# Kernel optimization log

Measured on AMD Instinct MI355X. Metric: run time of the kernel, lower is better.

## Reference

```python
import jax, jax.numpy as jnp
import numpy as np

COST_BBOX = 1.0
COST_GIOU = 1.0
TOPK = 5


def _make_boxes(key, b, n):
    # valid xyxy boxes in [0,1]: centers + small positive sizes
    kc, ks = jax.random.split(key)
    cxy = jax.random.uniform(kc, (b, n, 2))
    wh = jax.random.uniform(ks, (b, n, 2)) * 0.2 + 0.01
    return jnp.concatenate([cxy - wh / 2, cxy + wh / 2], axis=-1)


def setup_inputs() -> dict:
    key = jax.random.key(0)
    k1, k2, k3, k4 = jax.random.split(key, 4)
    B, NP, NG = 8, 5000, 300
    return {
        "pred_box": _make_boxes(k1, B, NP),
        "pred_obj": jax.random.normal(k3, (B, NP), dtype=jnp.float32),
        "gt_box": _make_boxes(k2, B, NG),
        "gt_obj": jax.random.normal(k4, (B, NG), dtype=jnp.float32),
    }


def pairwise_giou(pb, gb):
    # pb: [B,N,4], gb: [B,M,4] in xyxy -> giou [B,N,M]
    area_p = (pb[..., 2] - pb[..., 0]) * (pb[..., 3] - pb[..., 1])  # [B,N]
    area_g = (gb[..., 2] - gb[..., 0]) * (gb[..., 3] - gb[..., 1])  # [B,M]
    lt = jnp.maximum(pb[:, :, None, :2], gb[:, None, :, :2])  # [B,N,M,2]
    rb = jnp.minimum(pb[:, :, None, 2:], gb[:, None, :, 2:])
    wh = jnp.clip(rb - lt, 0.0)
    inter = wh[..., 0] * wh[..., 1]                                  # [B,N,M]
    union = area_p[:, :, None] + area_g[:, None, :] - inter
    iou = inter / union
    # smallest enclosing box
    lt_e = jnp.minimum(pb[:, :, None, :2], gb[:, None, :, :2])
    rb_e = jnp.maximum(pb[:, :, None, 2:], gb[:, None, :, 2:])
    wh_e = jnp.clip(rb_e - lt_e, 0.0)
    area_e = wh_e[..., 0] * wh_e[..., 1]
    return iou - (area_e - union) / area_e


def cost_matrix(pred_box, gt_box):
    # L1 cdist: [B,N,M]
    cost_bbox = jnp.sum(jnp.abs(pred_box[:, :, None, :] - gt_box[:, None, :, :]), axis=-1)
    cost_giou = 1.0 - pairwise_giou(pred_box, gt_box)
    return COST_BBOX * cost_bbox + COST_GIOU * cost_giou


def reference(pred_box, pred_obj, gt_box, gt_obj):
    C = cost_matrix(pred_box, gt_box)            # [B, N_pred, N_gt]
    Ct = jnp.swapaxes(C, 1, 2)                   # [B, N_gt, N_pred]
    _, idx = jax.lax.top_k(-Ct, TOPK)            # smallest-cost preds per gt: [B, N_gt, TOPK]
    B, M, _ = idx.shape
    matched_pred = idx.reshape(B, M * TOPK).astype(jnp.int32)
    matched_gt = jnp.broadcast_to(jnp.repeat(jnp.arange(M, dtype=jnp.int32), TOPK)[None, :], (B, M * TOPK))
    return matched_pred, matched_gt
```

## Files before the change

kernel.cpp:

```cpp
#include <hip/hip_runtime.h>

#pragma clang fp contract(off)

typedef unsigned long long u64;
typedef float f4 __attribute__((ext_vector_type(4)));

#define TOPK 5
#define WAVES 4

#define CE(x, y) do { const u64 _a = (x), _b = (y); const bool _l = _b < _a; \
                      (x) = _l ? _b : _a; (y) = _l ? _a : _b; } while (0)

__device__ __forceinline__ float fast_div(float a, float b) {
    float r = __builtin_amdgcn_rcpf(b);
    r = fmaf(fmaf(-b, r, 1.0f), r, r);
    float q = a * r;
    q = fmaf(fmaf(-b, q, a), r, q);
    return q;
}

__device__ __forceinline__ u64 eval_key(const f4 pb, const f4 gb,
                                        const float g_area, const int p) {
    const float area_p = (pb.z - pb.x) * (pb.w - pb.y);
    const float cost_bbox = fabsf(pb.x - gb.x) + fabsf(pb.y - gb.y)
                          + fabsf(pb.z - gb.z) + fabsf(pb.w - gb.w);
    const float ltx = fmaxf(pb.x, gb.x), lty = fmaxf(pb.y, gb.y);
    const float rbx = fminf(pb.z, gb.z), rby = fminf(pb.w, gb.w);
    const float iw = fmaxf(rbx - ltx, 0.0f), ih = fmaxf(rby - lty, 0.0f);
    const float inter = iw * ih;
    const float uni = area_p + g_area - inter;
    const float iou = fast_div(inter, uni);
    const float ex1 = fminf(pb.x, gb.x), ey1 = fminf(pb.y, gb.y);
    const float ex2 = fmaxf(pb.z, gb.z), ey2 = fmaxf(pb.w, gb.w);
    const float area_e = (ex2 - ex1) * (ey2 - ey1);
    const float giou = iou - fast_div(area_e - uni, area_e);
    const float cost = cost_bbox + (1.0f - giou);
    return ((u64)__float_as_uint(cost) << 32) | (unsigned)p;
}

__global__ __launch_bounds__(64 * WAVES) void matcher_topk_kernel(
    const float* __restrict__ pred_box,
    const float* __restrict__ gt_box,
    int* __restrict__ out_pred,
    int* __restrict__ out_gt,
    int B, int NP, int NG)
{
    const int pairsPerB = (NG + 1) >> 1;
    const int tp = blockIdx.x;
    const int b  = tp / pairsPerB;
    const int j  = tp - b * pairsPerB;
    const int m0 = 2 * j;
    const bool has1 = (m0 + 1 < NG);

    const int wid  = threadIdx.x >> 6;
    const int lane = threadIdx.x & 63;
    const int myGt = wid >> 1;
    const int half = wid & 1;

    const f4 gb = ((const f4*)gt_box)[b * NG + (myGt ? (has1 ? m0 + 1 : m0) : m0)];
    const float g_area = (gb.z - gb.x) * (gb.w - gb.y);

    const int NPm1  = NP - 1;
    const int hN    = (NP + 1) >> 1;
    const int start = half ? hN : 0;
    const int pend  = half ? NP : hN;
    int ngroups = (pend - start + 255) >> 8;
    ngroups += (ngroups & 1);

    u64 k0 = ~0ULL, k1 = ~0ULL, k2 = ~0ULL, k3 = ~0ULL, k4 = ~0ULL;

    const f4* pbase = (const f4*)pred_box + (size_t)b * NP;

#define GLOAD(g, rA, rB, rC, rD) do {                                        \
    const int _i = start + (g) * 256 + lane;                                 \
    const f4* _p0 = pbase + min(_i,       NPm1);                             \
    const f4* _p1 = pbase + min(_i + 64,  NPm1);                             \
    const f4* _p2 = pbase + min(_i + 128, NPm1);                             \
    const f4* _p3 = pbase + min(_i + 192, NPm1);                             \
    asm volatile("global_load_dwordx4 %0, %1, off" : "=v"(rA) : "v"(_p0));   \
    asm volatile("global_load_dwordx4 %0, %1, off" : "=v"(rB) : "v"(_p1));   \
    asm volatile("global_load_dwordx4 %0, %1, off" : "=v"(rC) : "v"(_p2));   \
    asm volatile("global_load_dwordx4 %0, %1, off" : "=v"(rD) : "v"(_p3));   \
} while (0)

#define GWAIT() do {                                   \
    asm volatile("s_waitcnt vmcnt(4)");                \
    __builtin_amdgcn_sched_barrier(0);                 \
} while (0)

#define PROCG(g, rA, rB, rC, rD) do {                                        \
    const int _i0 = start + (g) * 256 + lane;                                \
    u64 kA = eval_key(rA, gb, g_area, _i0);                                  \
    u64 kB = eval_key(rB, gb, g_area, _i0 + 64);                             \
    u64 kC = eval_key(rC, gb, g_area, _i0 + 128);                            \
    u64 kD = eval_key(rD, gb, g_area, _i0 + 192);                            \
    kA = (_i0       < pend) ? kA : ~0ULL;                                    \
    kB = (_i0 + 64  < pend) ? kB : ~0ULL;                                    \
    kC = (_i0 + 128 < pend) ? kC : ~0ULL;                                    \
    kD = (_i0 + 192 < pend) ? kD : ~0ULL;                                    \
    CE(kA, kB); CE(kC, kD); CE(kA, kC); CE(kB, kD); CE(kB, kC);              \
    u64 n0 = k0;                                                             \
    u64 n1 = k1 < kD ? k1 : kD;                                              \
    u64 n2 = k2 < kC ? k2 : kC;                                              \
    u64 n3 = k3 < kB ? k3 : kB;                                              \
    u64 n4 = k4 < kA ? k4 : kA;                                              \
    CE(n0, n1); CE(n3, n4); CE(n2, n4); CE(n2, n3); CE(n1, n4);              \
    CE(n0, n3); CE(n0, n2); CE(n1, n3); CE(n1, n2);                          \
    k0 = n0; k1 = n1; k2 = n2; k3 = n3; k4 = n4;                             \
} while (0)

    f4 eA, eB, eC, eD;
    f4 oA, oB, oC, oD;

    GLOAD(0, eA, eB, eC, eD);
    GLOAD(1, oA, oB, oC, oD);

    for (int g = 0; g < ngroups; g += 2) {
        GWAIT();
        PROCG(g, eA, eB, eC, eD);
        __builtin_amdgcn_sched_barrier(0);
        GLOAD(g + 2, eA, eB, eC, eD);
        GWAIT();
        PROCG(g + 1, oA, oB, oC, oD);
        __builtin_amdgcn_sched_barrier(0);
        GLOAD(g + 3, oA, oB, oC, oD);
    }

    asm volatile("s_waitcnt vmcnt(0)");
    __builtin_amdgcn_sched_barrier(0);
    asm volatile("" :: "v"(eA), "v"(eB), "v"(eC), "v"(eD),
                       "v"(oA), "v"(oB), "v"(oC), "v"(oD));

#undef GLOAD
#undef GWAIT
#undef PROCG

    #pragma unroll
    for (int off = 1; off < 64; off <<= 1) {
        const u64 b0 = __shfl_xor(k0, off);
        const u64 b1 = __shfl_xor(k1, off);
        const u64 b2 = __shfl_xor(k2, off);
        const u64 b3 = __shfl_xor(k3, off);
        const u64 b4 = __shfl_xor(k4, off);
        u64 m0_ = k0 < b4 ? k0 : b4;
        u64 m1_ = k1 < b3 ? k1 : b3;
        u64 m2_ = k2 < b2 ? k2 : b2;
        u64 m3_ = k3 < b1 ? k3 : b1;
        u64 m4_ = k4 < b0 ? k4 : b0;
        CE(m0_, m1_); CE(m3_, m4_); CE(m2_, m4_); CE(m2_, m3_); CE(m1_, m4_);
        CE(m0_, m3_); CE(m0_, m2_); CE(m1_, m3_); CE(m1_, m2_);
        k0 = m0_; k1 = m1_; k2 = m2_; k3 = m3_; k4 = m4_;
    }

    __shared__ u64 lds[WAVES][TOPK];
    if (lane == 0) {
        lds[wid][0] = k0; lds[wid][1] = k1; lds[wid][2] = k2;
        lds[wid][3] = k3; lds[wid][4] = k4;
    }
    __syncthreads();

    if (threadIdx.x < 2) {
        const int which = threadIdx.x;
        if (which == 0 || has1) {
            const int mm = m0 + which;
            int h0 = 0, h1 = 0;
            const int base = (b * NG + mm) * TOPK;
            #pragma unroll
            for (int r = 0; r < TOPK; ++r) {
                const u64 v0 = lds[which * 2][h0];
                const u64 v1 = lds[which * 2 + 1][h1];
                const bool t = v0 < v1;
                const u64 best = t ? v0 : v1;
                h0 += t; h1 += !t;
                out_pred[base + r] = (int)(unsigned)(best & 0xFFFFFFFFu);
                out_gt[base + r]   = mm;
            }
        }
    }
}

extern "C" void kernel_launch(void* const* d_in, const int* in_sizes, int n_in,
                              void* d_out, int out_size, void* d_ws, size_t ws_size,
                              hipStream_t stream) {
    const float* pred_box = (const float*)d_in[0];
    const float* gt_box   = (const float*)d_in[2];

    const int NP = 5000;
    const int B  = in_sizes[1] / NP;
    const int NG = in_sizes[3] / B;

    int* out_pred = (int*)d_out;
    int* out_gt   = out_pred + B * NG * TOPK;

    const int pairsPerB = (NG + 1) >> 1;
    const int blocks = B * pairsPerB;
    hipLaunchKernelGGL(matcher_topk_kernel, dim3(blocks), dim3(64 * WAVES), 0, stream,
                       pred_box, gt_box, out_pred, out_gt, B, NP, NG);
}
```

Before: 37.25 us.

## Assign one GT per block with all four waves splitting predictions

```diff
diff --git a/kernel.cpp b/kernel.cpp
--- a/kernel.cpp
+++ b/kernel.cpp
@@ -45,38 +45,29 @@
     int* __restrict__ out_gt,
     int B, int NP, int NG)
 {
-    const int pairsPerB = (NG + 1) >> 1;
-    const int tp = blockIdx.x;
-    const int b  = tp / pairsPerB;
-    const int j  = tp - b * pairsPerB;
-    const int m0 = 2 * j;
-    const bool has1 = (m0 + 1 < NG);
+    const int task = blockIdx.x;
+    const int t    = threadIdx.x;
+    const int wid  = t >> 6;
+    const int lane = t & 63;
+    const int b = task / NG;
+    const int m = task - b * NG;
 
-    const int wid  = threadIdx.x >> 6;
-    const int lane = threadIdx.x & 63;
-    const int myGt = wid >> 1;
-    const int half = wid & 1;
-
-    const f4 gb = ((const f4*)gt_box)[b * NG + (myGt ? (has1 ? m0 + 1 : m0) : m0)];
+    const f4 gb = ((const f4*)gt_box)[b * NG + m];
     const float g_area = (gb.z - gb.x) * (gb.w - gb.y);
 
-    const int NPm1  = NP - 1;
-    const int hN    = (NP + 1) >> 1;
-    const int start = half ? hN : 0;
-    const int pend  = half ? NP : hN;
-    int ngroups = (pend - start + 255) >> 8;
-    ngroups += (ngroups & 1);
+    const int NPm1    = NP - 1;
+    const int ngroups = (NP + 1023) >> 10;
 
     u64 k0 = ~0ULL, k1 = ~0ULL, k2 = ~0ULL, k3 = ~0ULL, k4 = ~0ULL;
 
     const f4* pbase = (const f4*)pred_box + (size_t)b * NP;
 
 #define GLOAD(g, rA, rB, rC, rD) do {                                        \
-    const int _i = start + (g) * 256 + lane;                                 \
+    const int _i = ((g) << 10) + t;                                          \
     const f4* _p0 = pbase + min(_i,       NPm1);                             \
-    const f4* _p1 = pbase + min(_i + 64,  NPm1);                             \
-    const f4* _p2 = pbase + min(_i + 128, NPm1);                             \
-    const f4* _p3 = pbase + min(_i + 192, NPm1);                             \
+    const f4* _p1 = pbase + min(_i + 256, NPm1);                             \
+    const f4* _p2 = pbase + min(_i + 512, NPm1);                             \
+    const f4* _p3 = pbase + min(_i + 768, NPm1);                             \
     asm volatile("global_load_dwordx4 %0, %1, off" : "=v"(rA) : "v"(_p0));   \
     asm volatile("global_load_dwordx4 %0, %1, off" : "=v"(rB) : "v"(_p1));   \
     asm volatile("global_load_dwordx4 %0, %1, off" : "=v"(rC) : "v"(_p2));   \
@@ -89,15 +80,15 @@
 } while (0)
 
 #define PROCG(g, rA, rB, rC, rD) do {                                        \
-    const int _i0 = start + (g) * 256 + lane;                                \
+    const int _i0 = ((g) << 10) + t;                                         \
     u64 kA = eval_key(rA, gb, g_area, _i0);                                  \
-    u64 kB = eval_key(rB, gb, g_area, _i0 + 64);                             \
-    u64 kC = eval_key(rC, gb, g_area, _i0 + 128);                            \
-    u64 kD = eval_key(rD, gb, g_area, _i0 + 192);                            \
-    kA = (_i0       < pend) ? kA : ~0ULL;                                    \
-    kB = (_i0 + 64  < pend) ? kB : ~0ULL;                                    \
-    kC = (_i0 + 128 < pend) ? kC : ~0ULL;                                    \
-    kD = (_i0 + 192 < pend) ? kD : ~0ULL;                                    \
+    u64 kB = eval_key(rB, gb, g_area, _i0 + 256);                            \
+    u64 kC = eval_key(rC, gb, g_area, _i0 + 512);                            \
+    u64 kD = eval_key(rD, gb, g_area, _i0 + 768);                            \
+    kA = (_i0       < NP) ? kA : ~0ULL;                                      \
+    kB = (_i0 + 256 < NP) ? kB : ~0ULL;                                      \
+    kC = (_i0 + 512 < NP) ? kC : ~0ULL;                                      \
+    kD = (_i0 + 768 < NP) ? kD : ~0ULL;                                      \
     CE(kA, kB); CE(kC, kD); CE(kA, kC); CE(kB, kD); CE(kB, kC);              \
     u64 n0 = k0;                                                             \
     u64 n1 = k1 < kD ? k1 : kD;                                              \
@@ -120,10 +111,12 @@
         PROCG(g, eA, eB, eC, eD);
         __builtin_amdgcn_sched_barrier(0);
         GLOAD(g + 2, eA, eB, eC, eD);
-        GWAIT();
-        PROCG(g + 1, oA, oB, oC, oD);
-        __builtin_amdgcn_sched_barrier(0);
-        GLOAD(g + 3, oA, oB, oC, oD);
+        if (g + 1 < ngroups) {
+            GWAIT();
+            PROCG(g + 1, oA, oB, oC, oD);
+            __builtin_amdgcn_sched_barrier(0);
+            GLOAD(g + 3, oA, oB, oC, oD);
+        }
     }
 
     asm volatile("s_waitcnt vmcnt(0)");
@@ -159,22 +152,22 @@
     }
     __syncthreads();
 
-    if (threadIdx.x < 2) {
-        const int which = threadIdx.x;
-        if (which == 0 || has1) {
-            const int mm = m0 + which;
-            int h0 = 0, h1 = 0;
-            const int base = (b * NG + mm) * TOPK;
+    if (t == 0) {
+        int head[WAVES];
+        #pragma unroll
+        for (int w = 0; w < WAVES; ++w) head[w] = 0;
+        const int baseo = task * TOPK;
+        #pragma unroll
+        for (int r = 0; r < TOPK; ++r) {
+            u64 best = ~0ULL; int bw = 0;
             #pragma unroll
-            for (int r = 0; r < TOPK; ++r) {
-                const u64 v0 = lds[which * 2][h0];
-                const u64 v1 = lds[which * 2 + 1][h1];
-                const bool t = v0 < v1;
-                const u64 best = t ? v0 : v1;
-                h0 += t; h1 += !t;
-                out_pred[base + r] = (int)(unsigned)(best & 0xFFFFFFFFu);
-                out_gt[base + r]   = mm;
+            for (int w = 0; w < WAVES; ++w) {
+                const u64 v = lds[w][head[w]];
+                if (v < best) { best = v; bw = w; }
             }
+            head[bw]++;
+            out_pred[baseo + r] = (int)(unsigned)(best & 0xFFFFFFFFu);
+            out_gt[baseo + r]   = m;
         }
     }
 }
@@ -192,8 +185,7 @@
     int* out_pred = (int*)d_out;
     int* out_gt   = out_pred + B * NG * TOPK;
 
-    const int pairsPerB = (NG + 1) >> 1;
-    const int blocks = B * pairsPerB;
-    hipLaunchKernelGGL(matcher_topk_kernel, dim3(blocks), dim3(64 * WAVES), 0, stream,
+    const int total = B * NG;
+    hipLaunchKernelGGL(matcher_topk_kernel, dim3(total), dim3(64 * WAVES), 0, stream,
                        pred_box, gt_box, out_pred, out_gt, B, NP, NG);
 }
```

New measurement: 42.78 us. +14.8%, slower.

## Assign one gt per wave over full pred range, drop LDS merge

Applied to the files above, without the earlier changes.

```diff
diff --git a/kernel.cpp b/kernel.cpp
--- a/kernel.cpp
+++ b/kernel.cpp
@@ -45,34 +45,29 @@
     int* __restrict__ out_gt,
     int B, int NP, int NG)
 {
-    const int pairsPerB = (NG + 1) >> 1;
+    const int quadsPerB = (NG + 3) >> 2;
     const int tp = blockIdx.x;
-    const int b  = tp / pairsPerB;
-    const int j  = tp - b * pairsPerB;
-    const int m0 = 2 * j;
-    const bool has1 = (m0 + 1 < NG);
+    const int b  = tp / quadsPerB;
+    const int j  = tp - b * quadsPerB;
 
     const int wid  = threadIdx.x >> 6;
     const int lane = threadIdx.x & 63;
-    const int myGt = wid >> 1;
-    const int half = wid & 1;
+    const int m = 4 * j + wid;
+    const bool active = (m < NG);
+    const int mm = active ? m : NG - 1;
 
-    const f4 gb = ((const f4*)gt_box)[b * NG + (myGt ? (has1 ? m0 + 1 : m0) : m0)];
+    const f4 gb = ((const f4*)gt_box)[b * NG + mm];
     const float g_area = (gb.z - gb.x) * (gb.w - gb.y);
 
-    const int NPm1  = NP - 1;
-    const int hN    = (NP + 1) >> 1;
-    const int start = half ? hN : 0;
-    const int pend  = half ? NP : hN;
-    int ngroups = (pend - start + 255) >> 8;
-    ngroups += (ngroups & 1);
+    const int NPm1    = NP - 1;
+    const int ngroups = (NP + 255) >> 8;
 
     u64 k0 = ~0ULL, k1 = ~0ULL, k2 = ~0ULL, k3 = ~0ULL, k4 = ~0ULL;
 
     const f4* pbase = (const f4*)pred_box + (size_t)b * NP;
 
 #define GLOAD(g, rA, rB, rC, rD) do {                                        \
-    const int _i = start + (g) * 256 + lane;                                 \
+    const int _i = ((g) << 8) + lane;                                        \
     const f4* _p0 = pbase + min(_i,       NPm1);                             \
     const f4* _p1 = pbase + min(_i + 64,  NPm1);                             \
     const f4* _p2 = pbase + min(_i + 128, NPm1);                             \
@@ -89,15 +84,17 @@
 } while (0)
 
 #define PROCG(g, rA, rB, rC, rD) do {                                        \
-    const int _i0 = start + (g) * 256 + lane;                                \
+    const int _i0 = ((g) << 8) + lane;                                       \
     u64 kA = eval_key(rA, gb, g_area, _i0);                                  \
     u64 kB = eval_key(rB, gb, g_area, _i0 + 64);                             \
     u64 kC = eval_key(rC, gb, g_area, _i0 + 128);                            \
     u64 kD = eval_key(rD, gb, g_area, _i0 + 192);                            \
-    kA = (_i0       < pend) ? kA : ~0ULL;                                    \
-    kB = (_i0 + 64  < pend) ? kB : ~0ULL;                                    \
-    kC = (_i0 + 128 < pend) ? kC : ~0ULL;                                    \
-    kD = (_i0 + 192 < pend) ? kD : ~0ULL;                                    \
+    if ((g) == ngroups - 1) {                  \
+        kA = (_i0       < NP) ? kA : ~0ULL;                                  \
+        kB = (_i0 + 64  < NP) ? kB : ~0ULL;                                  \
+        kC = (_i0 + 128 < NP) ? kC : ~0ULL;                                  \
+        kD = (_i0 + 192 < NP) ? kD : ~0ULL;                                  \
+    }                                                                        \
     CE(kA, kB); CE(kC, kD); CE(kA, kC); CE(kB, kD); CE(kB, kC);              \
     u64 n0 = k0;                                                             \
     u64 n1 = k1 < kD ? k1 : kD;                                              \
@@ -118,12 +115,12 @@
     for (int g = 0; g < ngroups; g += 2) {
         GWAIT();
         PROCG(g, eA, eB, eC, eD);
-        __builtin_amdgcn_sched_barrier(0);
         GLOAD(g + 2, eA, eB, eC, eD);
-        GWAIT();
-        PROCG(g + 1, oA, oB, oC, oD);
-        __builtin_amdgcn_sched_barrier(0);
-        GLOAD(g + 3, oA, oB, oC, oD);
+        if (g + 1 < ngroups) {
+            GWAIT();
+            PROCG(g + 1, oA, oB, oC, oD);
+            GLOAD(g + 3, oA, oB, oC, oD);
+        }
     }
 
     asm volatile("s_waitcnt vmcnt(0)");
@@ -152,30 +149,18 @@
         k0 = m0_; k1 = m1_; k2 = m2_; k3 = m3_; k4 = m4_;
     }
 
-    __shared__ u64 lds[WAVES][TOPK];
-    if (lane == 0) {
-        lds[wid][0] = k0; lds[wid][1] = k1; lds[wid][2] = k2;
-        lds[wid][3] = k3; lds[wid][4] = k4;
-    }
-    __syncthreads();
-
-    if (threadIdx.x < 2) {
-        const int which = threadIdx.x;
-        if (which == 0 || has1) {
-            const int mm = m0 + which;
-            int h0 = 0, h1 = 0;
-            const int base = (b * NG + mm) * TOPK;
-            #pragma unroll
-            for (int r = 0; r < TOPK; ++r) {
-                const u64 v0 = lds[which * 2][h0];
-                const u64 v1 = lds[which * 2 + 1][h1];
-                const bool t = v0 < v1;
-                const u64 best = t ? v0 : v1;
-                h0 += t; h1 += !t;
-                out_pred[base + r] = (int)(unsigned)(best & 0xFFFFFFFFu);
-                out_gt[base + r]   = mm;
-            }
-        }
+    if (active && lane == 0) {
+        const int baseo = (b * NG + m) * TOPK;
+        out_pred[baseo + 0] = (int)(unsigned)(k0 & 0xFFFFFFFFu);
+        out_pred[baseo + 1] = (int)(unsigned)(k1 & 0xFFFFFFFFu);
+        out_pred[baseo + 2] = (int)(unsigned)(k2 & 0xFFFFFFFFu);
+        out_pred[baseo + 3] = (int)(unsigned)(k3 & 0xFFFFFFFFu);
+        out_pred[baseo + 4] = (int)(unsigned)(k4 & 0xFFFFFFFFu);
+        out_gt[baseo + 0] = m;
+        out_gt[baseo + 1] = m;
+        out_gt[baseo + 2] = m;
+        out_gt[baseo + 3] = m;
+        out_gt[baseo + 4] = m;
     }
 }
 
@@ -192,8 +177,8 @@
     int* out_pred = (int*)d_out;
     int* out_gt   = out_pred + B * NG * TOPK;
 
-    const int pairsPerB = (NG + 1) >> 1;
-    const int blocks = B * pairsPerB;
+    const int quadsPerB = (NG + 3) >> 2;
+    const int blocks = B * quadsPerB;
     hipLaunchKernelGGL(matcher_topk_kernel, dim3(blocks), dim3(64 * WAVES), 0, stream,
                        pred_box, gt_box, out_pred, out_gt, B, NP, NG);
 }
```

Result: slower. 40.63 us (+9.1%).

## Fully unroll scan with triple-buffered prefetch and offset-based loads

Applied to the files above, without the earlier changes.

```diff
diff --git a/kernel.cpp b/kernel.cpp
--- a/kernel.cpp
+++ b/kernel.cpp
@@ -64,40 +64,48 @@
     const int hN    = (NP + 1) >> 1;
     const int start = half ? hN : 0;
     const int pend  = half ? NP : hN;
-    int ngroups = (pend - start + 255) >> 8;
-    ngroups += (ngroups & 1);
 
     u64 k0 = ~0ULL, k1 = ~0ULL, k2 = ~0ULL, k3 = ~0ULL, k4 = ~0ULL;
 
     const f4* pbase = (const f4*)pred_box + (size_t)b * NP;
 
-#define GLOAD(g, rA, rB, rC, rD) do {                                        \
-    const int _i = start + (g) * 256 + lane;                                 \
-    const f4* _p0 = pbase + min(_i,       NPm1);                             \
-    const f4* _p1 = pbase + min(_i + 64,  NPm1);                             \
-    const f4* _p2 = pbase + min(_i + 128, NPm1);                             \
-    const f4* _p3 = pbase + min(_i + 192, NPm1);                             \
-    asm volatile("global_load_dwordx4 %0, %1, off" : "=v"(rA) : "v"(_p0));   \
-    asm volatile("global_load_dwordx4 %0, %1, off" : "=v"(rB) : "v"(_p1));   \
-    asm volatile("global_load_dwordx4 %0, %1, off" : "=v"(rC) : "v"(_p2));   \
-    asm volatile("global_load_dwordx4 %0, %1, off" : "=v"(rD) : "v"(_p3));   \
-} while (0)
-
-#define GWAIT() do {                                   \
-    asm volatile("s_waitcnt vmcnt(4)");                \
-    __builtin_amdgcn_sched_barrier(0);                 \
-} while (0)
-
-#define PROCG(g, rA, rB, rC, rD) do {                                        \
-    const int _i0 = start + (g) * 256 + lane;                                \
+#define GLOADF(g, rA, rB, rC, rD) do {                                          \
+    const f4* _p = pbase + (start + ((g) << 8) + lane);                         \
+    asm volatile("global_load_dwordx4 %0, %1, off"             : "=v"(rA) : "v"(_p)); \
+    asm volatile("global_load_dwordx4 %0, %1, off offset:1024" : "=v"(rB) : "v"(_p)); \
+    asm volatile("global_load_dwordx4 %0, %1, off offset:2048" : "=v"(rC) : "v"(_p)); \
+    asm volatile("global_load_dwordx4 %0, %1, off offset:3072" : "=v"(rD) : "v"(_p)); \
+} while (0)
+
+#define GLOADS(g, rA, rB, rC, rD) do {                                          \
+    const int _i = start + ((g) << 8) + lane;                                   \
+    const f4* _p0 = pbase + min(_i,       NPm1);                                \
+    const f4* _p1 = pbase + min(_i + 64,  NPm1);                                \
+    const f4* _p2 = pbase + min(_i + 128, NPm1);                                \
+    const f4* _p3 = pbase + min(_i + 192, NPm1);                                \
+    asm volatile("global_load_dwordx4 %0, %1, off" : "=v"(rA) : "v"(_p0));      \
+    asm volatile("global_load_dwordx4 %0, %1, off" : "=v"(rB) : "v"(_p1));      \
+    asm volatile("global_load_dwordx4 %0, %1, off" : "=v"(rC) : "v"(_p2));      \
+    asm volatile("global_load_dwordx4 %0, %1, off" : "=v"(rD) : "v"(_p3));      \
+} while (0)
+
+#define W(n) do {                                         \
+    asm volatile("s_waitcnt vmcnt(" #n ")");              \
+    __builtin_amdgcn_sched_barrier(0);                    \
+} while (0)
+
+#define PROCG(g, TAIL, rA, rB, rC, rD) do {                                  \
+    const int _i0 = start + ((g) << 8) + lane;                               \
     u64 kA = eval_key(rA, gb, g_area, _i0);                                  \
     u64 kB = eval_key(rB, gb, g_area, _i0 + 64);                             \
     u64 kC = eval_key(rC, gb, g_area, _i0 + 128);                            \
     u64 kD = eval_key(rD, gb, g_area, _i0 + 192);                            \
-    kA = (_i0       < pend) ? kA : ~0ULL;                                    \
-    kB = (_i0 + 64  < pend) ? kB : ~0ULL;                                    \
-    kC = (_i0 + 128 < pend) ? kC : ~0ULL;                                    \
-    kD = (_i0 + 192 < pend) ? kD : ~0ULL;                                    \
+    if (TAIL) {                                                              \
+        kA = (_i0       < pend) ? kA : ~0ULL;                                \
+        kB = (_i0 + 64  < pend) ? kB : ~0ULL;                                \
+        kC = (_i0 + 128 < pend) ? kC : ~0ULL;                                \
+        kD = (_i0 + 192 < pend) ? kD : ~0ULL;                                \
+    }                                                                        \
     CE(kA, kB); CE(kC, kD); CE(kA, kC); CE(kB, kD); CE(kB, kC);              \
     u64 n0 = k0;                                                             \
     u64 n1 = k1 < kD ? k1 : kD;                                              \
@@ -109,30 +117,28 @@
     k0 = n0; k1 = n1; k2 = n2; k3 = n3; k4 = n4;                             \
 } while (0)
 
-    f4 eA, eB, eC, eD;
-    f4 oA, oB, oC, oD;
-
-    GLOAD(0, eA, eB, eC, eD);
-    GLOAD(1, oA, oB, oC, oD);
-
-    for (int g = 0; g < ngroups; g += 2) {
-        GWAIT();
-        PROCG(g, eA, eB, eC, eD);
-        __builtin_amdgcn_sched_barrier(0);
-        GLOAD(g + 2, eA, eB, eC, eD);
-        GWAIT();
-        PROCG(g + 1, oA, oB, oC, oD);
-        __builtin_amdgcn_sched_barrier(0);
-        GLOAD(g + 3, oA, oB, oC, oD);
-    }
-
-    asm volatile("s_waitcnt vmcnt(0)");
-    __builtin_amdgcn_sched_barrier(0);
-    asm volatile("" :: "v"(eA), "v"(eB), "v"(eC), "v"(eD),
-                       "v"(oA), "v"(oB), "v"(oC), "v"(oD));
-
-#undef GLOAD
-#undef GWAIT
+    f4 xA, xB, xC, xD;
+    f4 yA, yB, yC, yD;
+    f4 zA, zB, zC, zD;
+
+    GLOADF(0, xA, xB, xC, xD);
+    GLOADF(1, yA, yB, yC, yD);
+    GLOADF(2, zA, zB, zC, zD);
+
+    W(8); PROCG(0, false, xA, xB, xC, xD); GLOADF(3, xA, xB, xC, xD);
+    W(8); PROCG(1, false, yA, yB, yC, yD); GLOADF(4, yA, yB, yC, yD);
+    W(8); PROCG(2, false, zA, zB, zC, zD); GLOADF(5, zA, zB, zC, zD);
+    W(8); PROCG(3, false, xA, xB, xC, xD); GLOADF(6, xA, xB, xC, xD);
+    W(8); PROCG(4, false, yA, yB, yC, yD); GLOADF(7, yA, yB, yC, yD);
+    W(8); PROCG(5, false, zA, zB, zC, zD); GLOADF(8, zA, zB, zC, zD);
+    W(8); PROCG(6, false, xA, xB, xC, xD); GLOADS(9, xA, xB, xC, xD);
+    W(8); PROCG(7, false, yA, yB, yC, yD);
+    W(4); PROCG(8, false, zA, zB, zC, zD);
+    W(0); PROCG(9, true,  xA, xB, xC, xD);
+
+#undef GLOADF
+#undef GLOADS
+#undef W
 #undef PROCG
 
     #pragma unroll
```

Result: faster. 34.89 us (-6.3%).
